# Optimization experiments

Hardware: AMD Instinct MI355X
Metric: run time of the kernel (lower is better)

The kernel has to match this reference:

```python
import jax, jax.numpy as jnp
import numpy as np

L, B, E, H = 1024, 8, 1024, 16


def setup_inputs() -> dict:
    key = jax.random.key(0)
    k1, k2, k3, k4, k5 = jax.random.split(key, 5)
    scale = 1.0 / np.sqrt(E)
    return {
        "x": jax.random.normal(k1, (L, B, E), dtype=jnp.float32),
        "in_proj_weight": jax.random.normal(k2, (3 * E, E), dtype=jnp.float32) * scale,
        "in_proj_bias": jax.random.normal(k3, (3 * E,), dtype=jnp.float32) * 0.01,
        "out_proj_weight": jax.random.normal(k4, (E, E), dtype=jnp.float32) * scale,
        "out_proj_bias": jax.random.normal(k5, (E,), dtype=jnp.float32) * 0.01,
        "num_heads": H,
    }


def reference(x, in_proj_weight, in_proj_bias, out_proj_weight, out_proj_bias, num_heads):
    # x: [L, B, E] (tgt_len, batch, embed_dim), self-attention path of
    # multi_head_attention_func (no masks, no bias_k/v, no add_zero_attn,
    # dropout_p=0 / eval mode).
    Lq, Bq, Eq = x.shape
    hd = Eq // num_heads
    scaling = float(hd) ** -0.5
    # fused qkv projection: linear(x, in_proj_weight, in_proj_bias).chunk(3)
    qkv = x @ in_proj_weight.T + in_proj_bias  # [L, B, 3E]
    q, k, v = jnp.split(qkv, 3, axis=-1)
    q = q * scaling
    def to_heads(t):  # [L, B, E] -> [B*H, L, hd]
        return t.reshape(Lq, Bq * num_heads, hd).transpose(1, 0, 2)
    q, k, v = to_heads(q), to_heads(k), to_heads(v)
    # explicit QK^T -> softmax -> PV (naive attention, as in the source)
    scores = jnp.einsum('bqd,bkd->bqk', q, k)      # [B*H, L, L]
    attn = jax.nn.softmax(scores, axis=-1)
    out = jnp.einsum('bqk,bkd->bqd', attn, v)      # [B*H, L, hd]
    out = out.transpose(1, 0, 2).reshape(Lq, Bq, Eq)
    out = out @ out_proj_weight.T + out_proj_bias  # [L, B, E]
    return out
```

## Files before the change

### kernel.cpp

```cpp
#include <hip/hip_runtime.h>

#define L_DIM 1024
#define B_DIM 8
#define E_DIM 1024
#define H_DIM 16
#define HD 64
#define BH_DIM (B_DIM * H_DIM)

typedef float f32x4 __attribute__((ext_vector_type(4)));
typedef _Float16 f16_t;
typedef f16_t f16x4 __attribute__((ext_vector_type(4)));
typedef f16_t f16x8 __attribute__((ext_vector_type(8)));

static __device__ __forceinline__ void gld16(const void* g, void* l) {
  __builtin_amdgcn_global_load_lds(
      (const __attribute__((address_space(1))) unsigned int*)g,
      (__attribute__((address_space(3))) unsigned int*)l, 16, 0, 0);
}

__global__ __launch_bounds__(256) void convert_f16(
    const float* __restrict__ x, const float* __restrict__ wi,
    const float* __restrict__ wo, f16_t* __restrict__ x16,
    f16_t* __restrict__ wi16, f16_t* __restrict__ wo16) {
  const int NX = (L_DIM * B_DIM * E_DIM) / 4;
  const int NWI = (3 * E_DIM * E_DIM) / 4;
  const int NWO = (E_DIM * E_DIM) / 4;
  const int total = NX + NWI + NWO;
  for (int i = blockIdx.x * blockDim.x + threadIdx.x; i < total;
       i += gridDim.x * blockDim.x) {
    const float4* src; f16_t* dst; int j;
    if (i < NX)            { src = (const float4*)x;  dst = x16;  j = i; }
    else if (i < NX + NWI) { src = (const float4*)wi; dst = wi16; j = i - NX; }
    else                   { src = (const float4*)wo; dst = wo16; j = i - NX - NWI; }
    const float4 v = src[j];
    f16x4 h = {(f16_t)v.x, (f16_t)v.y, (f16_t)v.z, (f16_t)v.w};
    *(f16x4*)(dst + (size_t)j * 4) = h;
  }
}

template <int MODE>
__global__ __launch_bounds__(256, 2) void gemm_f16(
    const f16_t* __restrict__ A, const f16_t* __restrict__ B,
    const float* __restrict__ bias, void* __restrict__ O0v,
    void* __restrict__ O1v, void* __restrict__ O2v) {
  constexpr int K = 1024;
  __shared__ __align__(16) f16_t As[128 * 32];
  __shared__ __align__(16) f16_t Bs[128 * 32];

  const int tid = threadIdx.x;
  const int lane = tid & 63;
  const int wave = tid >> 6;
  const int wm = (wave & 1) * 64;
  const int wn = (wave >> 1) * 64;
  const int quad = lane >> 4;
  const int l16 = lane & 15;
  const int m0 = blockIdx.y * 128;
  const int n0 = blockIdx.x * 128;

  const int cr = tid >> 2;
  const int cc = (tid & 3) * 8;

  f32x4 acc[4][4] = {};

  for (int k0 = 0; k0 < K; k0 += 32) {
    __syncthreads();
    gld16(A + (size_t)(m0 + cr) * K + k0 + cc,      As + tid * 8);
    gld16(A + (size_t)(m0 + 64 + cr) * K + k0 + cc, As + 2048 + tid * 8);
    gld16(B + (size_t)(n0 + cr) * K + k0 + cc,      Bs + tid * 8);
    gld16(B + (size_t)(n0 + 64 + cr) * K + k0 + cc, Bs + 2048 + tid * 8);
    __syncthreads();

    f16x8 af[4], bf[4];
#pragma unroll
    for (int t = 0; t < 4; ++t) {
      af[t] = *(const f16x8*)&As[(wm + t * 16 + l16) * 32 + quad * 8];
      bf[t] = *(const f16x8*)&Bs[(wn + t * 16 + l16) * 32 + quad * 8];
    }
#pragma unroll
    for (int i = 0; i < 4; ++i)
#pragma unroll
      for (int j = 0; j < 4; ++j)
        acc[i][j] = __builtin_amdgcn_mfma_f32_16x16x32_f16(af[i], bf[j], acc[i][j], 0, 0, 0);
  }

#pragma unroll
  for (int i = 0; i < 4; ++i) {
    const int mbase = m0 + wm + i * 16 + quad * 4;
#pragma unroll
    for (int j = 0; j < 4; ++j) {
      const int n = n0 + wn + j * 16 + l16;
      const float bv = bias[n];
      if (MODE == 0) {
        f16_t* O0 = (f16_t*)O0v; f16_t* O1 = (f16_t*)O1v; f16_t* O2 = (f16_t*)O2v;
        const int chunk = n >> 10;
        const int e = n & 1023;
        const int h = e >> 6;
        const int d = e & 63;
#pragma unroll
        for (int r = 0; r < 4; ++r) {
          const int m = mbase + r;
          const int l = m >> 3, b = m & 7;
          const size_t idx = ((size_t)(b * H_DIM + h) * L_DIM + l) * HD + d;
          const float val = acc[i][j][r] + bv;
          if (chunk == 0)      O0[idx] = (f16_t)(val * 0.125f);
          else if (chunk == 1) O1[idx] = (f16_t)val;
          else                 O2[idx] = (f16_t)val;
        }
      } else {
        float* O0 = (float*)O0v;
#pragma unroll
        for (int r = 0; r < 4; ++r) {
          const int m = mbase + r;
          O0[(size_t)m * E_DIM + n] = acc[i][j][r] + bv;
        }
      }
    }
  }
}

__global__ __launch_bounds__(256) void vtrans(const f16_t* __restrict__ V,
                                              f16_t* __restrict__ Vt) {
  __shared__ f16_t T[64][72];
  const int bh = blockIdx.y;
  const int l0 = blockIdx.x * 64;
  const int t = threadIdx.x;
  const int r = t >> 3;
  const int c = (t & 7) * 8;
  const f16_t* src = V + ((size_t)bh * L_DIM + l0) * HD;
#pragma unroll
  for (int rr = 0; rr < 2; ++rr)
    *(f16x8*)&T[r + rr * 32][c] = *(const f16x8*)(src + (size_t)(r + rr * 32) * HD + c);
  __syncthreads();
#pragma unroll
  for (int rr = 0; rr < 2; ++rr) {
    const int d = r + rr * 32;
    f16x8 o;
#pragma unroll
    for (int j = 0; j < 8; ++j) o[j] = T[c + j][d];
    *(f16x8*)(Vt + ((size_t)bh * HD + d) * L_DIM + l0 + c) = o;
  }
}

__global__ __launch_bounds__(256, 4) void attn_f16(
    const f16_t* __restrict__ Q, const f16_t* __restrict__ K,
    const f16_t* __restrict__ Vt, f16_t* __restrict__ O) {
  constexpr int KSTR = 70;
  __shared__ __align__(16) f16_t Ks[64 * KSTR];
  __shared__ __align__(16) f16_t Vs[64 * KSTR];
  __shared__ float Ls[4][32];

  const int tid = threadIdx.x;
  const int lane = tid & 63;
  const int w = tid >> 6;
  const int quad = lane >> 4;
  const int l16 = lane & 15;
  const int bh = blockIdx.y;
  const int q0 = blockIdx.x * 128 + w * 32;

  const f16_t* Qb = Q + (size_t)bh * L_DIM * HD;
  const f16_t* Kb = K + (size_t)bh * L_DIM * HD;
  const f16_t* Vb = Vt + (size_t)bh * HD * L_DIM;

  f16x8 qf[2][2];
#pragma unroll
  for (int nt = 0; nt < 2; ++nt)
#pragma unroll
    for (int kc = 0; kc < 2; ++kc)
      qf[nt][kc] = *(const f16x8*)(Qb + (size_t)(q0 + nt * 16 + l16) * HD + kc * 32 + quad * 8);

  f32x4 oacc[2][4] = {};
  float rsum[2] = {0.0f, 0.0f};

  const int sr = tid >> 3;
  const int sc8 = (tid & 7) * 8;
  const int rA = (l16 >> 2) * 8 + (l16 & 3);

  for (int kt = 0; kt < 16; ++kt) {
    __syncthreads();
    {
      const f16_t* kp = Kb + (size_t)(kt * 64) * HD;
      const f16_t* vp = Vb + kt * 64;
#pragma unroll
      for (int rr = 0; rr < 2; ++rr) {
        const int row = sr + rr * 32;
        *(f16x8*)&Ks[row * KSTR + sc8] = *(const f16x8*)(kp + (size_t)row * HD + sc8);
        *(f16x8*)&Vs[row * KSTR + sc8] = *(const f16x8*)(vp + (size_t)row * L_DIM + sc8);
      }
    }
    __syncthreads();

    f32x4 sc[4][2] = {};
#pragma unroll
    for (int c = 0; c < 2; ++c)
#pragma unroll
      for (int h = 0; h < 2; ++h) {
        const int row = c * 32 + h * 4 + rA;
#pragma unroll
        for (int kc = 0; kc < 2; ++kc) {
          const f16x8 ka = *(const f16x8*)&Ks[row * KSTR + kc * 32 + quad * 8];
#pragma unroll
          for (int nt = 0; nt < 2; ++nt)
            sc[c * 2 + h][nt] =
                __builtin_amdgcn_mfma_f32_16x16x32_f16(ka, qf[nt][kc], sc[c * 2 + h][nt], 0, 0, 0);
        }
      }

    f16x8 pa[2][2];
#pragma unroll
    for (int c = 0; c < 2; ++c)
#pragma unroll
      for (int nt = 0; nt < 2; ++nt)
#pragma unroll
        for (int h = 0; h < 2; ++h)
#pragma unroll
          for (int r = 0; r < 4; ++r) {
            const float e = __expf(sc[c * 2 + h][nt][r]);
            rsum[nt] += e;
            pa[nt][c][h * 4 + r] = (f16_t)e;
          }

#pragma unroll
    for (int c = 0; c < 2; ++c)
#pragma unroll
      for (int nd = 0; nd < 4; ++nd) {
        const f16x8 vb = *(const f16x8*)&Vs[(nd * 16 + l16) * KSTR + c * 32 + quad * 8];
#pragma unroll
        for (int nt = 0; nt < 2; ++nt)
          oacc[nt][nd] =
              __builtin_amdgcn_mfma_f32_16x16x32_f16(pa[nt][c], vb, oacc[nt][nd], 0, 0, 0);
      }
  }

  float rs0 = rsum[0], rs1 = rsum[1];
  rs0 += __shfl_xor(rs0, 16); rs0 += __shfl_xor(rs0, 32);
  rs1 += __shfl_xor(rs1, 16); rs1 += __shfl_xor(rs1, 32);
  if (quad == 0) { Ls[w][l16] = rs0; Ls[w][16 + l16] = rs1; }
  asm volatile("s_waitcnt lgkmcnt(0)" ::: "memory");

  const int b = bh >> 4;
  const int h = bh & 15;
#pragma unroll
  for (int nt = 0; nt < 2; ++nt)
#pragma unroll
    for (int r = 0; r < 4; ++r) {
      const int ql = nt * 16 + quad * 4 + r;
      const float inv = 1.0f / Ls[w][ql];
      const int qrow = q0 + ql;
#pragma unroll
      for (int nd = 0; nd < 4; ++nd) {
        const int d = nd * 16 + l16;
        O[((size_t)qrow * B_DIM + b) * E_DIM + h * HD + d] = (f16_t)(oacc[nt][nd][r] * inv);
      }
    }
}

extern "C" void kernel_launch(void* const* d_in, const int* in_sizes, int n_in,
                              void* d_out, int out_size, void* d_ws, size_t ws_size,
                              hipStream_t stream) {
  const float* x     = (const float*)d_in[0];
  const float* w_in  = (const float*)d_in[1];
  const float* b_in  = (const float*)d_in[2];
  const float* w_out = (const float*)d_in[3];
  const float* b_out = (const float*)d_in[4];

  const size_t TS = (size_t)BH_DIM * L_DIM * HD;
  f16_t* q16  = (f16_t*)d_ws;
  f16_t* k16  = q16 + TS;
  f16_t* v16  = k16 + TS;
  f16_t* vt16 = v16 + TS;
  f16_t* x16  = vt16 + TS;
  f16_t* wi16 = x16 + TS;
  f16_t* wo16 = wi16 + (size_t)3 * E_DIM * E_DIM;
  f16_t* ao16 = x16;

  convert_f16<<<4096, 256, 0, stream>>>(x, w_in, w_out, x16, wi16, wo16);
  gemm_f16<0><<<dim3(24, 64), 256, 0, stream>>>(x16, wi16, b_in, q16, k16, v16);
  vtrans<<<dim3(16, 128), 256, 0, stream>>>(v16, vt16);
  attn_f16<<<dim3(8, 128), 256, 0, stream>>>(q16, k16, vt16, ao16);
  gemm_f16<1><<<dim3(8, 64), 256, 0, stream>>>(ao16, wo16, b_out, d_out, nullptr, nullptr);
}
```

Baseline: 259.7 us.

## Enlarge QKV GEMM N-tile and attention query tile per wave

The QKV projection GEMM becomes a dedicated kernel with a 128x256 block tile, so each wave computes 64x128 and reuses each A fragment across 8 B fragments. The attention kernel gives each wave 64 query rows instead of 32, doubling reuse of each K/V tile staged in LDS and halving the number of blocks. The score computation is restructured per 32-key chunk to limit live registers, and the occupancy hint is lowered to 2. The aim is to cut LDS and global traffic per FLOP, at the risk of higher register pressure and fewer resident waves.

```diff
diff --git a/kernel.cpp b/kernel.cpp
--- a/kernel.cpp
+++ b/kernel.cpp
@@ -38,11 +38,81 @@
   }
 }
 
-template <int MODE>
-__global__ __launch_bounds__(256, 2) void gemm_f16(
+__global__ __launch_bounds__(256, 2) void gemm_qkv(
     const f16_t* __restrict__ A, const f16_t* __restrict__ B,
-    const float* __restrict__ bias, void* __restrict__ O0v,
-    void* __restrict__ O1v, void* __restrict__ O2v) {
+    const float* __restrict__ bias, f16_t* __restrict__ O0,
+    f16_t* __restrict__ O1, f16_t* __restrict__ O2) {
+  constexpr int K = 1024;
+  __shared__ __align__(16) f16_t As[128 * 32];
+  __shared__ __align__(16) f16_t Bs[256 * 32];
+
+  const int tid = threadIdx.x;
+  const int lane = tid & 63;
+  const int wave = tid >> 6;
+  const int wm = (wave & 1) * 64;
+  const int wn = (wave >> 1) * 128;
+  const int quad = lane >> 4;
+  const int l16 = lane & 15;
+  const int m0 = blockIdx.y * 128;
+  const int n0 = blockIdx.x * 256;
+
+  const int cr = tid >> 2;
+  const int cc = (tid & 3) * 8;
+
+  f32x4 acc[4][8] = {};
+
+  for (int k0 = 0; k0 < K; k0 += 32) {
+    __syncthreads();
+    gld16(A + (size_t)(m0 + cr) * K + k0 + cc,        As + tid * 8);
+    gld16(A + (size_t)(m0 + 64 + cr) * K + k0 + cc,   As + 2048 + tid * 8);
+    gld16(B + (size_t)(n0 + cr) * K + k0 + cc,        Bs + tid * 8);
+    gld16(B + (size_t)(n0 + 64 + cr) * K + k0 + cc,   Bs + 2048 + tid * 8);
+    gld16(B + (size_t)(n0 + 128 + cr) * K + k0 + cc,  Bs + 4096 + tid * 8);
+    gld16(B + (size_t)(n0 + 192 + cr) * K + k0 + cc,  Bs + 6144 + tid * 8);
+    __syncthreads();
+
+    f16x8 af[4], bf[8];
+#pragma unroll
+    for (int t = 0; t < 4; ++t)
+      af[t] = *(const f16x8*)&As[(wm + t * 16 + l16) * 32 + quad * 8];
+#pragma unroll
+    for (int t = 0; t < 8; ++t)
+      bf[t] = *(const f16x8*)&Bs[(wn + t * 16 + l16) * 32 + quad * 8];
+#pragma unroll
+    for (int i = 0; i < 4; ++i)
+#pragma unroll
+      for (int j = 0; j < 8; ++j)
+        acc[i][j] = __builtin_amdgcn_mfma_f32_16x16x32_f16(af[i], bf[j], acc[i][j], 0, 0, 0);
+  }
+
+#pragma unroll
+  for (int i = 0; i < 4; ++i) {
+    const int mbase = m0 + wm + i * 16 + quad * 4;
+#pragma unroll
+    for (int j = 0; j < 8; ++j) {
+      const int n = n0 + wn + j * 16 + l16;
+      const float bv = bias[n];
+      const int chunk = n >> 10;
+      const int e = n & 1023;
+      const int h = e >> 6;
+      const int d = e & 63;
+#pragma unroll
+      for (int r = 0; r < 4; ++r) {
+        const int m = mbase + r;
+        const int l = m >> 3, b = m & 7;
+        const size_t idx = ((size_t)(b * H_DIM + h) * L_DIM + l) * HD + d;
+        const float val = acc[i][j][r] + bv;
+        if (chunk == 0)      O0[idx] = (f16_t)(val * 0.125f);
+        else if (chunk == 1) O1[idx] = (f16_t)val;
+        else                 O2[idx] = (f16_t)val;
+      }
+    }
+  }
+}
+
+__global__ __launch_bounds__(256, 2) void gemm_out(
+    const f16_t* __restrict__ A, const f16_t* __restrict__ B,
+    const float* __restrict__ bias, float* __restrict__ O) {
   constexpr int K = 1024;
   __shared__ __align__(16) f16_t As[128 * 32];
   __shared__ __align__(16) f16_t Bs[128 * 32];
@@ -90,30 +160,9 @@
     for (int j = 0; j < 4; ++j) {
       const int n = n0 + wn + j * 16 + l16;
       const float bv = bias[n];
-      if (MODE == 0) {
-        f16_t* O0 = (f16_t*)O0v; f16_t* O1 = (f16_t*)O1v; f16_t* O2 = (f16_t*)O2v;
-        const int chunk = n >> 10;
-        const int e = n & 1023;
-        const int h = e >> 6;
-        const int d = e & 63;
-#pragma unroll
-        for (int r = 0; r < 4; ++r) {
-          const int m = mbase + r;
-          const int l = m >> 3, b = m & 7;
-          const size_t idx = ((size_t)(b * H_DIM + h) * L_DIM + l) * HD + d;
-          const float val = acc[i][j][r] + bv;
-          if (chunk == 0)      O0[idx] = (f16_t)(val * 0.125f);
-          else if (chunk == 1) O1[idx] = (f16_t)val;
-          else                 O2[idx] = (f16_t)val;
-        }
-      } else {
-        float* O0 = (float*)O0v;
-#pragma unroll
-        for (int r = 0; r < 4; ++r) {
-          const int m = mbase + r;
-          O0[(size_t)m * E_DIM + n] = acc[i][j][r] + bv;
-        }
-      }
+#pragma unroll
+      for (int r = 0; r < 4; ++r)
+        O[(size_t)(mbase + r) * E_DIM + n] = acc[i][j][r] + bv;
     }
   }
 }
@@ -141,13 +190,13 @@
   }
 }
 
-__global__ __launch_bounds__(256, 4) void attn_f16(
+__global__ __launch_bounds__(256, 2) void attn_f16(
     const f16_t* __restrict__ Q, const f16_t* __restrict__ K,
     const f16_t* __restrict__ Vt, f16_t* __restrict__ O) {
   constexpr int KSTR = 70;
   __shared__ __align__(16) f16_t Ks[64 * KSTR];
   __shared__ __align__(16) f16_t Vs[64 * KSTR];
-  __shared__ float Ls[4][32];
+  __shared__ float Ls[4][64];
 
   const int tid = threadIdx.x;
   const int lane = tid & 63;
@@ -155,21 +204,21 @@
   const int quad = lane >> 4;
   const int l16 = lane & 15;
   const int bh = blockIdx.y;
-  const int q0 = blockIdx.x * 128 + w * 32;
+  const int q0 = blockIdx.x * 256 + w * 64;
 
   const f16_t* Qb = Q + (size_t)bh * L_DIM * HD;
   const f16_t* Kb = K + (size_t)bh * L_DIM * HD;
   const f16_t* Vb = Vt + (size_t)bh * HD * L_DIM;
 
-  f16x8 qf[2][2];
-#pragma unroll
-  for (int nt = 0; nt < 2; ++nt)
+  f16x8 qf[4][2];
+#pragma unroll
+  for (int nt = 0; nt < 4; ++nt)
 #pragma unroll
     for (int kc = 0; kc < 2; ++kc)
       qf[nt][kc] = *(const f16x8*)(Qb + (size_t)(q0 + nt * 16 + l16) * HD + kc * 32 + quad * 8);
 
-  f32x4 oacc[2][4] = {};
-  float rsum[2] = {0.0f, 0.0f};
+  f32x4 oacc[4][4] = {};
+  float rsum[4] = {0.0f, 0.0f, 0.0f, 0.0f};
 
   const int sr = tid >> 3;
   const int sc8 = (tid & 7) * 8;
@@ -189,9 +238,9 @@
     }
     __syncthreads();
 
-    f32x4 sc[4][2] = {};
-#pragma unroll
-    for (int c = 0; c < 2; ++c)
+#pragma unroll
+    for (int c = 0; c < 2; ++c) {
+      f32x4 sc[2][4] = {};
 #pragma unroll
       for (int h = 0; h < 2; ++h) {
         const int row = c * 32 + h * 4 + rA;
@@ -199,48 +248,45 @@
         for (int kc = 0; kc < 2; ++kc) {
           const f16x8 ka = *(const f16x8*)&Ks[row * KSTR + kc * 32 + quad * 8];
 #pragma unroll
-          for (int nt = 0; nt < 2; ++nt)
-            sc[c * 2 + h][nt] =
-                __builtin_amdgcn_mfma_f32_16x16x32_f16(ka, qf[nt][kc], sc[c * 2 + h][nt], 0, 0, 0);
+          for (int nt = 0; nt < 4; ++nt)
+            sc[h][nt] = __builtin_amdgcn_mfma_f32_16x16x32_f16(ka, qf[nt][kc], sc[h][nt], 0, 0, 0);
         }
       }
 
-    f16x8 pa[2][2];
-#pragma unroll
-    for (int c = 0; c < 2; ++c)
-#pragma unroll
-      for (int nt = 0; nt < 2; ++nt)
+      f16x8 pa[4];
+#pragma unroll
+      for (int nt = 0; nt < 4; ++nt)
 #pragma unroll
         for (int h = 0; h < 2; ++h)
 #pragma unroll
           for (int r = 0; r < 4; ++r) {
-            const float e = __expf(sc[c * 2 + h][nt][r]);
+            const float e = __expf(sc[h][nt][r]);
             rsum[nt] += e;
-            pa[nt][c][h * 4 + r] = (f16_t)e;
+            pa[nt][h * 4 + r] = (f16_t)e;
           }
 
-#pragma unroll
-    for (int c = 0; c < 2; ++c)
 #pragma unroll
       for (int nd = 0; nd < 4; ++nd) {
         const f16x8 vb = *(const f16x8*)&Vs[(nd * 16 + l16) * KSTR + c * 32 + quad * 8];
 #pragma unroll
-        for (int nt = 0; nt < 2; ++nt)
-          oacc[nt][nd] =
-              __builtin_amdgcn_mfma_f32_16x16x32_f16(pa[nt][c], vb, oacc[nt][nd], 0, 0, 0);
-      }
-  }
-
-  float rs0 = rsum[0], rs1 = rsum[1];
-  rs0 += __shfl_xor(rs0, 16); rs0 += __shfl_xor(rs0, 32);
-  rs1 += __shfl_xor(rs1, 16); rs1 += __shfl_xor(rs1, 32);
-  if (quad == 0) { Ls[w][l16] = rs0; Ls[w][16 + l16] = rs1; }
+        for (int nt = 0; nt < 4; ++nt)
+          oacc[nt][nd] = __builtin_amdgcn_mfma_f32_16x16x32_f16(pa[nt], vb, oacc[nt][nd], 0, 0, 0);
+      }
+    }
+  }
+
+#pragma unroll
+  for (int nt = 0; nt < 4; ++nt) {
+    float rs = rsum[nt];
+    rs += __shfl_xor(rs, 16); rs += __shfl_xor(rs, 32);
+    if (quad == 0) Ls[w][nt * 16 + l16] = rs;
+  }
   asm volatile("s_waitcnt lgkmcnt(0)" ::: "memory");
 
   const int b = bh >> 4;
   const int h = bh & 15;
 #pragma unroll
-  for (int nt = 0; nt < 2; ++nt)
+  for (int nt = 0; nt < 4; ++nt)
 #pragma unroll
     for (int r = 0; r < 4; ++r) {
       const int ql = nt * 16 + quad * 4 + r;
@@ -274,8 +320,8 @@
   f16_t* ao16 = x16;
 
   convert_f16<<<4096, 256, 0, stream>>>(x, w_in, w_out, x16, wi16, wo16);
-  gemm_f16<0><<<dim3(24, 64), 256, 0, stream>>>(x16, wi16, b_in, q16, k16, v16);
+  gemm_qkv<<<dim3(12, 64), 256, 0, stream>>>(x16, wi16, b_in, q16, k16, v16);
   vtrans<<<dim3(16, 128), 256, 0, stream>>>(v16, vt16);
-  attn_f16<<<dim3(8, 128), 256, 0, stream>>>(q16, k16, vt16, ao16);
-  gemm_f16<1><<<dim3(8, 64), 256, 0, stream>>>(ao16, wo16, b_out, d_out, nullptr, nullptr);
-}
+  attn_f16<<<dim3(4, 128), 256, 0, stream>>>(q16, k16, vt16, ao16);
+  gemm_out<<<dim3(8, 64), 256, 0, stream>>>(ao16, wo16, b_out, (float*)d_out);
+}
```

After: 255.2 us. No clear change (-1.7%).

## Fuse V transpose into attention and double query rows per wave

Applied to the files above, without the earlier changes.

Drops the separate vtrans kernel. The attention kernel now reads V in its original [L, hd] layout and transposes it on the fly while staging into LDS, using 32-bit loads and half-word shuffles. Each wave now handles 64 query rows instead of 32, which halves the grid and doubles K/V reuse per LDS tile. The cost is higher register pressure (launch bounds lowered to 2), fewer blocks (512), and narrower uncoalesced 4-byte V loads.

```diff
diff --git a/kernel.cpp b/kernel.cpp
--- a/kernel.cpp
+++ b/kernel.cpp
@@ -118,36 +118,13 @@
   }
 }
 
-__global__ __launch_bounds__(256) void vtrans(const f16_t* __restrict__ V,
-                                              f16_t* __restrict__ Vt) {
-  __shared__ f16_t T[64][72];
-  const int bh = blockIdx.y;
-  const int l0 = blockIdx.x * 64;
-  const int t = threadIdx.x;
-  const int r = t >> 3;
-  const int c = (t & 7) * 8;
-  const f16_t* src = V + ((size_t)bh * L_DIM + l0) * HD;
-#pragma unroll
-  for (int rr = 0; rr < 2; ++rr)
-    *(f16x8*)&T[r + rr * 32][c] = *(const f16x8*)(src + (size_t)(r + rr * 32) * HD + c);
-  __syncthreads();
-#pragma unroll
-  for (int rr = 0; rr < 2; ++rr) {
-    const int d = r + rr * 32;
-    f16x8 o;
-#pragma unroll
-    for (int j = 0; j < 8; ++j) o[j] = T[c + j][d];
-    *(f16x8*)(Vt + ((size_t)bh * HD + d) * L_DIM + l0 + c) = o;
-  }
-}
-
-__global__ __launch_bounds__(256, 4) void attn_f16(
+__global__ __launch_bounds__(256, 2) void attn_f16(
     const f16_t* __restrict__ Q, const f16_t* __restrict__ K,
-    const f16_t* __restrict__ Vt, f16_t* __restrict__ O) {
+    const f16_t* __restrict__ V, f16_t* __restrict__ O) {
   constexpr int KSTR = 70;
   __shared__ __align__(16) f16_t Ks[64 * KSTR];
   __shared__ __align__(16) f16_t Vs[64 * KSTR];
-  __shared__ float Ls[4][32];
+  __shared__ float Ls[4][64];
 
   const int tid = threadIdx.x;
   const int lane = tid & 63;
@@ -155,43 +132,55 @@
   const int quad = lane >> 4;
   const int l16 = lane & 15;
   const int bh = blockIdx.y;
-  const int q0 = blockIdx.x * 128 + w * 32;
+  const int q0 = blockIdx.x * 256 + w * 64;
 
   const f16_t* Qb = Q + (size_t)bh * L_DIM * HD;
   const f16_t* Kb = K + (size_t)bh * L_DIM * HD;
-  const f16_t* Vb = Vt + (size_t)bh * HD * L_DIM;
-
-  f16x8 qf[2][2];
-#pragma unroll
-  for (int nt = 0; nt < 2; ++nt)
+  const f16_t* Vb = V + (size_t)bh * L_DIM * HD;
+
+  f16x8 qf[4][2];
+#pragma unroll
+  for (int nt = 0; nt < 4; ++nt)
 #pragma unroll
     for (int kc = 0; kc < 2; ++kc)
       qf[nt][kc] = *(const f16x8*)(Qb + (size_t)(q0 + nt * 16 + l16) * HD + kc * 32 + quad * 8);
 
-  f32x4 oacc[2][4] = {};
-  float rsum[2] = {0.0f, 0.0f};
+  f32x4 oacc[4][4] = {};
+  float rsum[4] = {0.0f, 0.0f, 0.0f, 0.0f};
 
   const int sr = tid >> 3;
   const int sc8 = (tid & 7) * 8;
+  const int va = tid & 31;
+  const int vg = tid >> 5;
   const int rA = (l16 >> 2) * 8 + (l16 & 3);
 
   for (int kt = 0; kt < 16; ++kt) {
     __syncthreads();
     {
       const f16_t* kp = Kb + (size_t)(kt * 64) * HD;
-      const f16_t* vp = Vb + kt * 64;
 #pragma unroll
       for (int rr = 0; rr < 2; ++rr) {
         const int row = sr + rr * 32;
         *(f16x8*)&Ks[row * KSTR + sc8] = *(const f16x8*)(kp + (size_t)row * HD + sc8);
-        *(f16x8*)&Vs[row * KSTR + sc8] = *(const f16x8*)(vp + (size_t)row * L_DIM + sc8);
-      }
-    }
-    __syncthreads();
-
-    f32x4 sc[4][2] = {};
-#pragma unroll
-    for (int c = 0; c < 2; ++c)
+      }
+      const f16_t* vp = Vb + (size_t)(kt * 64 + vg * 8) * HD + 2 * va;
+      unsigned int vd[8];
+#pragma unroll
+      for (int i = 0; i < 8; ++i) vd[i] = *(const unsigned int*)(vp + (size_t)i * HD);
+      union { unsigned int u[4]; f16x8 v; } lo, hi;
+#pragma unroll
+      for (int i = 0; i < 4; ++i) {
+        lo.u[i] = (vd[2 * i] & 0xffffu) | (vd[2 * i + 1] << 16);
+        hi.u[i] = (vd[2 * i] >> 16) | (vd[2 * i + 1] & 0xffff0000u);
+      }
+      *(f16x8*)&Vs[(2 * va) * KSTR + vg * 8] = lo.v;
+      *(f16x8*)&Vs[(2 * va + 1) * KSTR + vg * 8] = hi.v;
+    }
+    __syncthreads();
+
+#pragma unroll
+    for (int c = 0; c < 2; ++c) {
+      f32x4 sc[2][4] = {};
 #pragma unroll
       for (int h = 0; h < 2; ++h) {
         const int row = c * 32 + h * 4 + rA;
@@ -199,48 +188,45 @@
         for (int kc = 0; kc < 2; ++kc) {
           const f16x8 ka = *(const f16x8*)&Ks[row * KSTR + kc * 32 + quad * 8];
 #pragma unroll
-          for (int nt = 0; nt < 2; ++nt)
-            sc[c * 2 + h][nt] =
-                __builtin_amdgcn_mfma_f32_16x16x32_f16(ka, qf[nt][kc], sc[c * 2 + h][nt], 0, 0, 0);
+          for (int nt = 0; nt < 4; ++nt)
+            sc[h][nt] = __builtin_amdgcn_mfma_f32_16x16x32_f16(ka, qf[nt][kc], sc[h][nt], 0, 0, 0);
         }
       }
 
-    f16x8 pa[2][2];
-#pragma unroll
-    for (int c = 0; c < 2; ++c)
-#pragma unroll
-      for (int nt = 0; nt < 2; ++nt)
+      f16x8 pa[4];
+#pragma unroll
+      for (int nt = 0; nt < 4; ++nt)
 #pragma unroll
         for (int h = 0; h < 2; ++h)
 #pragma unroll
           for (int r = 0; r < 4; ++r) {
-            const float e = __expf(sc[c * 2 + h][nt][r]);
+            const float e = __expf(sc[h][nt][r]);
             rsum[nt] += e;
-            pa[nt][c][h * 4 + r] = (f16_t)e;
+            pa[nt][h * 4 + r] = (f16_t)e;
           }
 
-#pragma unroll
-    for (int c = 0; c < 2; ++c)
 #pragma unroll
       for (int nd = 0; nd < 4; ++nd) {
         const f16x8 vb = *(const f16x8*)&Vs[(nd * 16 + l16) * KSTR + c * 32 + quad * 8];
 #pragma unroll
-        for (int nt = 0; nt < 2; ++nt)
-          oacc[nt][nd] =
-              __builtin_amdgcn_mfma_f32_16x16x32_f16(pa[nt][c], vb, oacc[nt][nd], 0, 0, 0);
-      }
-  }
-
-  float rs0 = rsum[0], rs1 = rsum[1];
-  rs0 += __shfl_xor(rs0, 16); rs0 += __shfl_xor(rs0, 32);
-  rs1 += __shfl_xor(rs1, 16); rs1 += __shfl_xor(rs1, 32);
-  if (quad == 0) { Ls[w][l16] = rs0; Ls[w][16 + l16] = rs1; }
+        for (int nt = 0; nt < 4; ++nt)
+          oacc[nt][nd] = __builtin_amdgcn_mfma_f32_16x16x32_f16(pa[nt], vb, oacc[nt][nd], 0, 0, 0);
+      }
+    }
+  }
+
+#pragma unroll
+  for (int nt = 0; nt < 4; ++nt) {
+    float rs = rsum[nt];
+    rs += __shfl_xor(rs, 16); rs += __shfl_xor(rs, 32);
+    if (quad == 0) Ls[w][nt * 16 + l16] = rs;
+  }
   asm volatile("s_waitcnt lgkmcnt(0)" ::: "memory");
 
   const int b = bh >> 4;
   const int h = bh & 15;
 #pragma unroll
-  for (int nt = 0; nt < 2; ++nt)
+  for (int nt = 0; nt < 4; ++nt)
 #pragma unroll
     for (int r = 0; r < 4; ++r) {
       const int ql = nt * 16 + quad * 4 + r;
@@ -267,15 +253,13 @@
   f16_t* q16  = (f16_t*)d_ws;
   f16_t* k16  = q16 + TS;
   f16_t* v16  = k16 + TS;
-  f16_t* vt16 = v16 + TS;
-  f16_t* x16  = vt16 + TS;
+  f16_t* x16  = v16 + TS;
   f16_t* wi16 = x16 + TS;
   f16_t* wo16 = wi16 + (size_t)3 * E_DIM * E_DIM;
   f16_t* ao16 = x16;
 
   convert_f16<<<4096, 256, 0, stream>>>(x, w_in, w_out, x16, wi16, wo16);
   gemm_f16<0><<<dim3(24, 64), 256, 0, stream>>>(x16, wi16, b_in, q16, k16, v16);
-  vtrans<<<dim3(16, 128), 256, 0, stream>>>(v16, vt16);
-  attn_f16<<<dim3(8, 128), 256, 0, stream>>>(q16, k16, vt16, ao16);
+  attn_f16<<<dim3(4, 128), 256, 0, stream>>>(q16, k16, v16, ao16);
   gemm_f16<1><<<dim3(8, 64), 256, 0, stream>>>(ao16, wo16, b_out, d_out, nullptr, nullptr);
 }
```

Measured after the change: 240.4 us. 7.4% less time.
